# Optimization experiments

Measured on AMD Instinct MI355X. Metric: run time of the kernel, lower is better.

The kernel has to match this reference:

```python
import jax, jax.numpy as jnp
import numpy as np

N_E = 4096
E_DIM = 512
BETA = 0.25


def setup_inputs() -> dict:
    key = jax.random.key(0)
    k1, k2 = jax.random.split(key)
    z = jax.random.normal(k1, (32, 512, E_DIM), dtype=jnp.float32)
    # embedding.weight ~ U(-1/n_e, 1/n_e)
    emb = jax.random.uniform(k2, (N_E, E_DIM), dtype=jnp.float32,
                             minval=-1.0 / N_E, maxval=1.0 / N_E)
    return {"z": z, "emb": emb}


def reference(z, emb):
    B, S, D = z.shape
    zf = z.reshape(-1, D)  # (N, D)
    # squared L2 distances: ||z||^2 + ||e||^2 - 2 z @ e^T  -> (N, n_e)
    d = (jnp.sum(zf * zf, axis=1, keepdims=True)
         + jnp.sum(emb * emb, axis=1)
         - 2.0 * jnp.matmul(zf, emb.T))
    idx = jnp.argmin(d, axis=1)  # (N,)
    z_q = emb[idx].reshape(z.shape)

    # commitment / codebook loss (detach = stop_gradient)
    loss = (jnp.mean((z_q - jax.lax.stop_gradient(z)) ** 2)
            + BETA * jnp.mean((jax.lax.stop_gradient(z_q) - z) ** 2))

    # straight-through estimator
    z_q_st = z + jax.lax.stop_gradient(z_q - z)

    # perplexity via codeword usage histogram (equiv. to mean of one-hots)
    N = zf.shape[0]
    counts = jnp.zeros((N_E,), dtype=z.dtype).at[idx].add(1.0)
    e_mean = counts / N
    perplexity = jnp.exp(-jnp.sum(e_mean * jnp.log(e_mean + 1e-10)))

    return (loss, z_q_st, idx, perplexity)
```

## Files before the change

kernel.cpp:

```cpp
#include <hip/hip_runtime.h>
#include <math.h>

#define NROWS 16384
#define DDIM  512
#define NE    4096
#define NZ    (NROWS * DDIM)
#define MAXC  32
#define MARGIN 2e-3f

typedef __attribute__((ext_vector_type(8))) short bf16x8;
typedef __attribute__((ext_vector_type(4))) float f32x4;

__device__ __forceinline__ float sqr_rn(float x) { return __fmul_rn(x, x); }
__device__ __forceinline__ ushort f2bf(float f) {
    const unsigned u = __float_as_uint(f);
    return (ushort)((u + 0x7fffu + ((u >> 16) & 1u)) >> 16);
}
__device__ __forceinline__ unsigned pack2(float a, float b) {
    return (unsigned)f2bf(a) | ((unsigned)f2bf(b) << 16);
}

__global__ void k_prepZ(const float* __restrict__ z, ushort* __restrict__ zh,
                        float* __restrict__ znorm) {
    const int t = blockIdx.x * blockDim.x + threadIdx.x;
    const int row = t >> 2, blk = t & 3;
    const float4* p = (const float4*)(z + (size_t)row * DDIM + blk * 128);
    ushort* zo = zh + (size_t)row * DDIM + blk * 128;
    float4 v0 = p[0], v1 = p[1];
    {
        uint4 w; w.x = pack2(v0.x, v0.y); w.y = pack2(v0.z, v0.w);
        w.z = pack2(v1.x, v1.y); w.w = pack2(v1.z, v1.w);
        *(uint4*)zo = w;
    }
    float r[8];
    r[0] = sqr_rn(v0.x); r[1] = sqr_rn(v0.y); r[2] = sqr_rn(v0.z); r[3] = sqr_rn(v0.w);
    r[4] = sqr_rn(v1.x); r[5] = sqr_rn(v1.y); r[6] = sqr_rn(v1.z); r[7] = sqr_rn(v1.w);
    #pragma unroll
    for (int i = 1; i < 16; ++i) {
        v0 = p[2 * i]; v1 = p[2 * i + 1];
        uint4 w; w.x = pack2(v0.x, v0.y); w.y = pack2(v0.z, v0.w);
        w.z = pack2(v1.x, v1.y); w.w = pack2(v1.z, v1.w);
        *(uint4*)(zo + i * 8) = w;
        r[0] = __fadd_rn(r[0], sqr_rn(v0.x)); r[1] = __fadd_rn(r[1], sqr_rn(v0.y));
        r[2] = __fadd_rn(r[2], sqr_rn(v0.z)); r[3] = __fadd_rn(r[3], sqr_rn(v0.w));
        r[4] = __fadd_rn(r[4], sqr_rn(v1.x)); r[5] = __fadd_rn(r[5], sqr_rn(v1.y));
        r[6] = __fadd_rn(r[6], sqr_rn(v1.z)); r[7] = __fadd_rn(r[7], sqr_rn(v1.w));
    }
    const float B = __fadd_rn(__fadd_rn(__fadd_rn(r[0], r[1]), __fadd_rn(r[2], r[3])),
                              __fadd_rn(__fadd_rn(r[4], r[5]), __fadd_rn(r[6], r[7])));
    const float s01 = __fadd_rn(B, __shfl_xor(B, 1));
    const float zn  = __fadd_rn(s01, __shfl_xor(s01, 2));
    if (blk == 0) znorm[row] = zn;
}

__global__ void k_prepE(const float* __restrict__ emb, ushort* __restrict__ eh,
                        float* __restrict__ bnorm, unsigned* __restrict__ counts) {
    const int lane = threadIdx.x & 63;
    const int c = (blockIdx.x * blockDim.x + threadIdx.x) >> 6;
    const float4* p = (const float4*)(emb + (size_t)c * DDIM);
    const float4 v0 = p[lane * 2], v1 = p[lane * 2 + 1];
    uint4 w; w.x = pack2(v0.x, v0.y); w.y = pack2(v0.z, v0.w);
    w.z = pack2(v1.x, v1.y); w.w = pack2(v1.z, v1.w);
    *(uint4*)(eh + (size_t)c * DDIM + lane * 8) = w;
    float s = v0.x*v0.x + v0.y*v0.y + v0.z*v0.z + v0.w*v0.w
            + v1.x*v1.x + v1.y*v1.y + v1.z*v1.z + v1.w*v1.w;
    #pragma unroll
    for (int m = 32; m; m >>= 1) s += __shfl_xor(s, m);
    if (lane == 0) { bnorm[c] = s; counts[c] = 0u; }
}

__global__ __launch_bounds__(256) void k_mfma(const ushort* __restrict__ zh,
                                              const ushort* __restrict__ eh,
                                              const float* __restrict__ bnorm,
                                              ushort* __restrict__ sbuf) {
    __shared__ ushort Af[8 * 512];
    __shared__ ushort Bf[8 * 512];
    const int tid = threadIdx.x;
    const int lane = tid & 63;
    const int w = tid >> 6;
    const int wrow = (w >> 1) * 64, wcol = (w & 1) * 64;
    const int rbase = blockIdx.x * 128, cbase = blockIdx.y * 128;
    const int sr = tid >> 1, sh = tid & 1;
    const int g  = sr >> 4, r15 = sr & 15;
    const int r16 = lane & 15, g4 = (lane >> 4) * 4;

    f32x4 acc[4][4];
    #pragma unroll
    for (int i = 0; i < 4; ++i)
        #pragma unroll
        for (int j = 0; j < 4; ++j) acc[i][j] = (f32x4){0.f, 0.f, 0.f, 0.f};

    for (int kb = 0; kb < DDIM; kb += 32) {
        const ushort* ga = zh + (size_t)(rbase + sr) * DDIM + kb + sh * 16;
        const ushort* gb = eh + (size_t)(cbase + sr) * DDIM + kb + sh * 16;
        const uint4 qa0 = *(const uint4*)ga;
        const uint4 qa1 = *(const uint4*)(ga + 8);
        const uint4 qb0 = *(const uint4*)gb;
        const uint4 qb1 = *(const uint4*)(gb + 8);
        __syncthreads();
        {
            ushort* pa = &Af[g * 512 + r15 * 8 + sh * 4];
            *(uint2*)(pa +   0) = make_uint2(qa0.x, qa0.y);
            *(uint2*)(pa + 128) = make_uint2(qa0.z, qa0.w);
            *(uint2*)(pa + 256) = make_uint2(qa1.x, qa1.y);
            *(uint2*)(pa + 384) = make_uint2(qa1.z, qa1.w);
            ushort* pb = &Bf[g * 512 + r15 * 8 + sh * 4];
            *(uint2*)(pb +   0) = make_uint2(qb0.x, qb0.y);
            *(uint2*)(pb + 128) = make_uint2(qb0.z, qb0.w);
            *(uint2*)(pb + 256) = make_uint2(qb1.x, qb1.y);
            *(uint2*)(pb + 384) = make_uint2(qb1.z, qb1.w);
        }
        __syncthreads();
        bf16x8 af[4], bf[4];
        #pragma unroll
        for (int f = 0; f < 4; ++f) {
            af[f] = *(const bf16x8*)&Af[((wrow >> 4) + f) * 512 + lane * 8];
            bf[f] = *(const bf16x8*)&Bf[((wcol >> 4) + f) * 512 + lane * 8];
        }
        #pragma unroll
        for (int fi = 0; fi < 4; ++fi)
            #pragma unroll
            for (int fj = 0; fj < 4; ++fj)
                acc[fi][fj] = __builtin_amdgcn_mfma_f32_16x16x32_bf16(
                    af[fi], bf[fj], acc[fi][fj], 0, 0, 0);
    }

    float bn[4];
    #pragma unroll
    for (int fj = 0; fj < 4; ++fj) bn[fj] = bnorm[cbase + wcol + fj * 16 + r16];

    #pragma unroll
    for (int fi = 0; fi < 4; ++fi) {
        #pragma unroll
        for (int r = 0; r < 4; ++r) {
            const int row = rbase + wrow + fi * 16 + g4 + r;
            float s[4];
            #pragma unroll
            for (int fj = 0; fj < 4; ++fj) s[fj] = fmaf(-2.f, acc[fi][fj][r], bn[fj]);
            uint2* sp = (uint2*)(sbuf + (size_t)row * NE + cbase + wcol);
            sp[r16] = make_uint2(pack2(s[0], s[1]), pack2(s[2], s[3]));
        }
    }
}

__device__ __forceinline__ unsigned long long exact_key(const float4* __restrict__ zp4,
                                                        const float* __restrict__ emb,
                                                        const float* __restrict__ bnorm,
                                                        float zn, int c) {
    const float4* ep4 = (const float4*)(emb + (size_t)c * DDIM);
    float acc = 0.f;
    #pragma unroll 8
    for (int q = 0; q < DDIM / 4; ++q) {
        const float4 zv = zp4[q];
        const float4 ev = ep4[q];
        acc = fmaf(zv.x, ev.x, acc);
        acc = fmaf(zv.y, ev.y, acc);
        acc = fmaf(zv.z, ev.z, acc);
        acc = fmaf(zv.w, ev.w, acc);
    }
    const float s = __fsub_rn(__fadd_rn(zn, bnorm[c]), __fmul_rn(2.f, acc));
    return ((unsigned long long)__float_as_uint(s) << 32) | (unsigned)c;
}

__global__ void k_pick(const ushort* __restrict__ sbuf, const float* __restrict__ z,
                       const float* __restrict__ emb, const float* __restrict__ znorm,
                       const float* __restrict__ bnorm, int* __restrict__ idxbuf) {
    __shared__ unsigned candL[4][MAXC];
    __shared__ unsigned cntL[4];
    const int lane = threadIdx.x & 63;
    const int w = threadIdx.x >> 6;
    const int row = blockIdx.x * 4 + w;
    if (threadIdx.x < 4) cntL[threadIdx.x] = 0u;
    __syncthreads();

    const uint4* p = (const uint4*)(sbuf + (size_t)row * NE);
    uint4 v[8];
    #pragma unroll
    for (int j = 0; j < 8; ++j) v[j] = p[j * 64 + lane];
    float mn = INFINITY;
    #pragma unroll
    for (int j = 0; j < 8; ++j) {
        const unsigned* u = (const unsigned*)&v[j];
        #pragma unroll
        for (int q = 0; q < 4; ++q) {
            mn = fminf(mn, __uint_as_float(u[q] << 16));
            mn = fminf(mn, __uint_as_float(u[q] & 0xffff0000u));
        }
    }
    #pragma unroll
    for (int m = 32; m; m >>= 1) mn = fminf(mn, __shfl_xor(mn, m));
    const float thr = mn + MARGIN;
    #pragma unroll
    for (int j = 0; j < 8; ++j) {
        const unsigned* u = (const unsigned*)&v[j];
        #pragma unroll
        for (int q = 0; q < 4; ++q) {
            #pragma unroll
            for (int hi = 0; hi < 2; ++hi) {
                const float val = __uint_as_float(hi ? (u[q] & 0xffff0000u) : (u[q] << 16));
                if (val <= thr) {
                    const int pos = j * 512 + lane * 8 + q * 2 + hi;
                    const int inb = pos & 63;
                    const int col = (pos >> 6) * 64 + (inb & 3) * 16 + (inb >> 2);
                    const unsigned slot = atomicAdd(&cntL[w], 1u);
                    if (slot < MAXC) candL[w][slot] = (unsigned)col;
                }
            }
        }
    }
    __syncthreads();

    const int cnt = (int)cntL[w];
    int id;
    if (cnt == 1) {
        id = (int)(candL[w][0] & (NE - 1));
    } else {
        const float zn = znorm[row];
        const float4* zp4 = (const float4*)(z + (size_t)row * DDIM);
        unsigned long long best = ~0ULL;
        if (cnt >= 2 && cnt <= MAXC) {
            if (lane < cnt)
                best = exact_key(zp4, emb, bnorm, zn, (int)(candL[w][lane] & (NE - 1)));
        } else {
            for (int c = lane; c < NE; c += 64) {
                const unsigned long long k = exact_key(zp4, emb, bnorm, zn, c);
                if (k < best) best = k;
            }
        }
        #pragma unroll
        for (int m = 32; m; m >>= 1) {
            const unsigned long long ov = __shfl_xor(best, m);
            if (ov < best) best = ov;
        }
        id = (int)(__shfl(best, 0) & (unsigned long long)(NE - 1));
    }
    if (lane == 0) idxbuf[row] = id;
}

__global__ void k_gather(const int* __restrict__ idxbuf, const float* __restrict__ z,
                         const float* __restrict__ emb, float* __restrict__ out,
                         unsigned* __restrict__ counts, float* __restrict__ d2buf) {
    const int lane = threadIdx.x & 63;
    const int row = blockIdx.x * 4 + (threadIdx.x >> 6);
    const int id = idxbuf[row] & (NE - 1);
    const float* zp = z + (size_t)row * DDIM;
    const float* ep = emb + (size_t)id * DDIM;
    float* op = out + 1 + (size_t)row * DDIM;
    float d2 = 0.f;
    #pragma unroll
    for (int m = 0; m < 8; ++m) {
        const int k = m * 64 + lane;
        const float e = ep[k];
        const float zv = zp[k];
        const float t = e - zv;
        op[k] = zv + t;
        d2 = fmaf(t, t, d2);
    }
    #pragma unroll
    for (int m = 32; m; m >>= 1) d2 += __shfl_xor(d2, m);
    if (lane == 0) {
        atomicAdd(&counts[id], 1u);
        d2buf[row] = d2;
        out[1 + (size_t)NZ + row] = (float)id;
    }
}

__global__ void k_final(const float* __restrict__ d2buf, const unsigned* __restrict__ counts,
                        float* __restrict__ out) {
    __shared__ double sh[256];
    __shared__ float  shf[256];
    const int tid = threadIdx.x;
    double ent = 0.0;
    for (int i = tid; i < NE; i += 256) {
        const double p = (double)counts[i] / (double)NROWS;
        ent += p * log(p + 1e-10);
    }
    float sse = 0.f;
    for (int i = tid; i < NROWS; i += 256) sse += d2buf[i];
    sh[tid] = ent; shf[tid] = sse;
    __syncthreads();
    for (int s = 128; s; s >>= 1) {
        if (tid < s) { sh[tid] += sh[tid + s]; shf[tid] += shf[tid + s]; }
        __syncthreads();
    }
    if (tid == 0) {
        out[0] = 1.25f * (shf[0] / (float)NZ);
        out[1 + (size_t)NZ + NROWS] = (float)exp(-sh[0]);
    }
}

extern "C" void kernel_launch(void* const* d_in, const int* in_sizes, int n_in,
                              void* d_out, int out_size, void* d_ws, size_t ws_size,
                              hipStream_t stream) {
    const float* z   = (const float*)d_in[0];
    const float* emb = (const float*)d_in[1];
    float* out = (float*)d_out;
    char* ws = (char*)d_ws;

    ushort* zh = (ushort*)(out + 4);
    ushort* eh = (ushort*)(out + 4 + 4194304);

    size_t off = 0;
    float*    bnorm  = (float*)(ws + off); off += (size_t)NE * 4;
    unsigned* counts = (unsigned*)(ws + off); off += (size_t)NE * 4;
    float*    d2buf  = (float*)(ws + off); off += (size_t)NROWS * 4;
    float*    znorm  = (float*)(ws + off); off += (size_t)NROWS * 4;
    int*      idxbuf = (int*)(ws + off); off += (size_t)NROWS * 4;
    ushort*   sbuf   = (ushort*)(ws + off);

    k_prepZ<<<256, 256, 0, stream>>>(z, zh, znorm);
    k_prepE<<<1024, 256, 0, stream>>>(emb, eh, bnorm, counts);
    k_mfma<<<dim3(NROWS / 128, NE / 128), 256, 0, stream>>>(zh, eh, bnorm, sbuf);
    k_pick<<<NROWS / 4, 256, 0, stream>>>(sbuf, z, emb, znorm, bnorm, idxbuf);
    k_gather<<<NROWS / 4, 256, 0, stream>>>(idxbuf, z, emb, out, counts, d2buf);
    k_final<<<1, 256, 0, stream>>>(d2buf, counts, out);
}
```

Before: 296.3 us.

## Fuse prep kernels, use global_load_lds in MFMA, add block-min guided pick

Merges the z and codebook prep kernels into one launch and fuses pick with gather, which drops the idx buffer round trip. The MFMA kernel now loads tiles straight from global memory into LDS with global_load_lds instead of staging them through registers. It also writes a per-row, per-64-column block minimum, so the pick kernel only rescans blocks within the margin instead of reading the whole bf16 score row. This adds extra writes and shuffles in the MFMA epilogue, raises the candidate cap to 64, and falls back to the old path when the workspace is too small.

```diff
diff --git a/kernel.cpp b/kernel.cpp
--- a/kernel.cpp
+++ b/kernel.cpp
@@ -5,7 +5,7 @@
 #define DDIM  512
 #define NE    4096
 #define NZ    (NROWS * DDIM)
-#define MAXC  32
+#define MAXC  64
 #define MARGIN 2e-3f
 
 typedef __attribute__((ext_vector_type(8))) short bf16x8;
@@ -19,60 +19,68 @@
 __device__ __forceinline__ unsigned pack2(float a, float b) {
     return (unsigned)f2bf(a) | ((unsigned)f2bf(b) << 16);
 }
-
-__global__ void k_prepZ(const float* __restrict__ z, ushort* __restrict__ zh,
-                        float* __restrict__ znorm) {
-    const int t = blockIdx.x * blockDim.x + threadIdx.x;
-    const int row = t >> 2, blk = t & 3;
-    const float4* p = (const float4*)(z + (size_t)row * DDIM + blk * 128);
-    ushort* zo = zh + (size_t)row * DDIM + blk * 128;
-    float4 v0 = p[0], v1 = p[1];
-    {
+__device__ __forceinline__ void glds16(const void* g, void* l) {
+    __builtin_amdgcn_global_load_lds(
+        (const __attribute__((address_space(1))) unsigned int*)g,
+        (__attribute__((address_space(3))) unsigned int*)l, 16, 0, 0);
+}
+
+__global__ void k_prep(const float* __restrict__ z, const float* __restrict__ emb,
+                       ushort* __restrict__ zh, ushort* __restrict__ eh,
+                       float* __restrict__ znorm, float* __restrict__ bnorm,
+                       unsigned* __restrict__ counts) {
+    if (blockIdx.x < 1024) {
+        const int lane = threadIdx.x & 63;
+        const int c = (int)((blockIdx.x * 256 + threadIdx.x) >> 6);
+        const float4* p = (const float4*)(emb + (size_t)c * DDIM);
+        const float4 v0 = p[lane * 2], v1 = p[lane * 2 + 1];
         uint4 w; w.x = pack2(v0.x, v0.y); w.y = pack2(v0.z, v0.w);
         w.z = pack2(v1.x, v1.y); w.w = pack2(v1.z, v1.w);
-        *(uint4*)zo = w;
-    }
-    float r[8];
-    r[0] = sqr_rn(v0.x); r[1] = sqr_rn(v0.y); r[2] = sqr_rn(v0.z); r[3] = sqr_rn(v0.w);
-    r[4] = sqr_rn(v1.x); r[5] = sqr_rn(v1.y); r[6] = sqr_rn(v1.z); r[7] = sqr_rn(v1.w);
-    #pragma unroll
-    for (int i = 1; i < 16; ++i) {
-        v0 = p[2 * i]; v1 = p[2 * i + 1];
-        uint4 w; w.x = pack2(v0.x, v0.y); w.y = pack2(v0.z, v0.w);
-        w.z = pack2(v1.x, v1.y); w.w = pack2(v1.z, v1.w);
-        *(uint4*)(zo + i * 8) = w;
-        r[0] = __fadd_rn(r[0], sqr_rn(v0.x)); r[1] = __fadd_rn(r[1], sqr_rn(v0.y));
-        r[2] = __fadd_rn(r[2], sqr_rn(v0.z)); r[3] = __fadd_rn(r[3], sqr_rn(v0.w));
-        r[4] = __fadd_rn(r[4], sqr_rn(v1.x)); r[5] = __fadd_rn(r[5], sqr_rn(v1.y));
-        r[6] = __fadd_rn(r[6], sqr_rn(v1.z)); r[7] = __fadd_rn(r[7], sqr_rn(v1.w));
-    }
-    const float B = __fadd_rn(__fadd_rn(__fadd_rn(r[0], r[1]), __fadd_rn(r[2], r[3])),
-                              __fadd_rn(__fadd_rn(r[4], r[5]), __fadd_rn(r[6], r[7])));
-    const float s01 = __fadd_rn(B, __shfl_xor(B, 1));
-    const float zn  = __fadd_rn(s01, __shfl_xor(s01, 2));
-    if (blk == 0) znorm[row] = zn;
-}
-
-__global__ void k_prepE(const float* __restrict__ emb, ushort* __restrict__ eh,
-                        float* __restrict__ bnorm, unsigned* __restrict__ counts) {
-    const int lane = threadIdx.x & 63;
-    const int c = (blockIdx.x * blockDim.x + threadIdx.x) >> 6;
-    const float4* p = (const float4*)(emb + (size_t)c * DDIM);
-    const float4 v0 = p[lane * 2], v1 = p[lane * 2 + 1];
-    uint4 w; w.x = pack2(v0.x, v0.y); w.y = pack2(v0.z, v0.w);
-    w.z = pack2(v1.x, v1.y); w.w = pack2(v1.z, v1.w);
-    *(uint4*)(eh + (size_t)c * DDIM + lane * 8) = w;
-    float s = v0.x*v0.x + v0.y*v0.y + v0.z*v0.z + v0.w*v0.w
-            + v1.x*v1.x + v1.y*v1.y + v1.z*v1.z + v1.w*v1.w;
-    #pragma unroll
-    for (int m = 32; m; m >>= 1) s += __shfl_xor(s, m);
-    if (lane == 0) { bnorm[c] = s; counts[c] = 0u; }
-}
-
+        *(uint4*)(eh + (size_t)c * DDIM + lane * 8) = w;
+        float s = v0.x*v0.x + v0.y*v0.y + v0.z*v0.z + v0.w*v0.w
+                + v1.x*v1.x + v1.y*v1.y + v1.z*v1.z + v1.w*v1.w;
+        #pragma unroll
+        for (int m = 32; m; m >>= 1) s += __shfl_xor(s, m);
+        if (lane == 0) { bnorm[c] = s; counts[c] = 0u; }
+    } else {
+        const int t = (int)((blockIdx.x - 1024) * 256 + threadIdx.x);
+        const int row = t >> 2, blk = t & 3;
+        const float4* p = (const float4*)(z + (size_t)row * DDIM + blk * 128);
+        ushort* zo = zh + (size_t)row * DDIM + blk * 128;
+        float4 v0 = p[0], v1 = p[1];
+        {
+            uint4 w; w.x = pack2(v0.x, v0.y); w.y = pack2(v0.z, v0.w);
+            w.z = pack2(v1.x, v1.y); w.w = pack2(v1.z, v1.w);
+            *(uint4*)zo = w;
+        }
+        float r[8];
+        r[0] = sqr_rn(v0.x); r[1] = sqr_rn(v0.y); r[2] = sqr_rn(v0.z); r[3] = sqr_rn(v0.w);
+        r[4] = sqr_rn(v1.x); r[5] = sqr_rn(v1.y); r[6] = sqr_rn(v1.z); r[7] = sqr_rn(v1.w);
+        #pragma unroll
+        for (int i = 1; i < 16; ++i) {
+            v0 = p[2 * i]; v1 = p[2 * i + 1];
+            uint4 w; w.x = pack2(v0.x, v0.y); w.y = pack2(v0.z, v0.w);
+            w.z = pack2(v1.x, v1.y); w.w = pack2(v1.z, v1.w);
+            *(uint4*)(zo + i * 8) = w;
+            r[0] = __fadd_rn(r[0], sqr_rn(v0.x)); r[1] = __fadd_rn(r[1], sqr_rn(v0.y));
+            r[2] = __fadd_rn(r[2], sqr_rn(v0.z)); r[3] = __fadd_rn(r[3], sqr_rn(v0.w));
+            r[4] = __fadd_rn(r[4], sqr_rn(v1.x)); r[5] = __fadd_rn(r[5], sqr_rn(v1.y));
+            r[6] = __fadd_rn(r[6], sqr_rn(v1.z)); r[7] = __fadd_rn(r[7], sqr_rn(v1.w));
+        }
+        const float B = __fadd_rn(__fadd_rn(__fadd_rn(r[0], r[1]), __fadd_rn(r[2], r[3])),
+                                  __fadd_rn(__fadd_rn(r[4], r[5]), __fadd_rn(r[6], r[7])));
+        const float s01 = __fadd_rn(B, __shfl_xor(B, 1));
+        const float zn  = __fadd_rn(s01, __shfl_xor(s01, 2));
+        if (blk == 0) znorm[row] = zn;
+    }
+}
+
+template <int USE_BLK>
 __global__ __launch_bounds__(256) void k_mfma(const ushort* __restrict__ zh,
                                               const ushort* __restrict__ eh,
                                               const float* __restrict__ bnorm,
-                                              ushort* __restrict__ sbuf) {
+                                              ushort* __restrict__ sbuf,
+                                              float* __restrict__ rowblkmin) {
     __shared__ ushort Af[8 * 512];
     __shared__ ushort Bf[8 * 512];
     const int tid = threadIdx.x;
@@ -80,9 +88,16 @@
     const int w = tid >> 6;
     const int wrow = (w >> 1) * 64, wcol = (w & 1) * 64;
     const int rbase = blockIdx.x * 128, cbase = blockIdx.y * 128;
-    const int sr = tid >> 1, sh = tid & 1;
-    const int g  = sr >> 4, r15 = sr & 15;
     const int r16 = lane & 15, g4 = (lane >> 4) * 4;
+    const int k8 = (lane >> 4) * 8;
+    const int c0 = 2 * w, c1 = c0 + 1;
+
+    const ushort* gA0 = zh + (size_t)(rbase + 16 * c0 + r16) * DDIM + k8;
+    const ushort* gA1 = zh + (size_t)(rbase + 16 * c1 + r16) * DDIM + k8;
+    const ushort* gB0 = eh + (size_t)(cbase + 16 * c0 + r16) * DDIM + k8;
+    const ushort* gB1 = eh + (size_t)(cbase + 16 * c1 + r16) * DDIM + k8;
+    ushort* lA0 = &Af[c0 * 512]; ushort* lA1 = &Af[c1 * 512];
+    ushort* lB0 = &Bf[c0 * 512]; ushort* lB1 = &Bf[c1 * 512];
 
     f32x4 acc[4][4];
     #pragma unroll
@@ -91,25 +106,11 @@
         for (int j = 0; j < 4; ++j) acc[i][j] = (f32x4){0.f, 0.f, 0.f, 0.f};
 
     for (int kb = 0; kb < DDIM; kb += 32) {
-        const ushort* ga = zh + (size_t)(rbase + sr) * DDIM + kb + sh * 16;
-        const ushort* gb = eh + (size_t)(cbase + sr) * DDIM + kb + sh * 16;
-        const uint4 qa0 = *(const uint4*)ga;
-        const uint4 qa1 = *(const uint4*)(ga + 8);
-        const uint4 qb0 = *(const uint4*)gb;
-        const uint4 qb1 = *(const uint4*)(gb + 8);
         __syncthreads();
-        {
-            ushort* pa = &Af[g * 512 + r15 * 8 + sh * 4];
-            *(uint2*)(pa +   0) = make_uint2(qa0.x, qa0.y);
-            *(uint2*)(pa + 128) = make_uint2(qa0.z, qa0.w);
-            *(uint2*)(pa + 256) = make_uint2(qa1.x, qa1.y);
-            *(uint2*)(pa + 384) = make_uint2(qa1.z, qa1.w);
-            ushort* pb = &Bf[g * 512 + r15 * 8 + sh * 4];
-            *(uint2*)(pb +   0) = make_uint2(qb0.x, qb0.y);
-            *(uint2*)(pb + 128) = make_uint2(qb0.z, qb0.w);
-            *(uint2*)(pb + 256) = make_uint2(qb1.x, qb1.y);
-            *(uint2*)(pb + 384) = make_uint2(qb1.z, qb1.w);
-        }
+        glds16(gA0 + kb, lA0);
+        glds16(gA1 + kb, lA1);
+        glds16(gB0 + kb, lB0);
+        glds16(gB1 + kb, lB1);
         __syncthreads();
         bf16x8 af[4], bf[4];
         #pragma unroll
@@ -139,6 +140,13 @@
             for (int fj = 0; fj < 4; ++fj) s[fj] = fmaf(-2.f, acc[fi][fj][r], bn[fj]);
             uint2* sp = (uint2*)(sbuf + (size_t)row * NE + cbase + wcol);
             sp[r16] = make_uint2(pack2(s[0], s[1]), pack2(s[2], s[3]));
+            if (USE_BLK) {
+                float m = fminf(fminf(s[0], s[1]), fminf(s[2], s[3]));
+                #pragma unroll
+                for (int x = 1; x < 16; x <<= 1) m = fminf(m, __shfl_xor(m, x));
+                if (r16 == 0)
+                    rowblkmin[(size_t)row * 64 + blockIdx.y * 2 + (w & 1)] = m;
+            }
         }
     }
 }
@@ -162,10 +170,13 @@
     return ((unsigned long long)__float_as_uint(s) << 32) | (unsigned)c;
 }
 
-__global__ void k_pick(const ushort* __restrict__ sbuf, const float* __restrict__ z,
-                       const float* __restrict__ emb, const float* __restrict__ znorm,
-                       const float* __restrict__ bnorm, int* __restrict__ idxbuf) {
-    __shared__ unsigned candL[4][MAXC];
+template <int GUIDED>
+__global__ void k_pg(const ushort* __restrict__ sbuf, const float* __restrict__ rowblkmin,
+                     const float* __restrict__ z, const float* __restrict__ emb,
+                     const float* __restrict__ znorm, const float* __restrict__ bnorm,
+                     float* __restrict__ out, unsigned* __restrict__ counts,
+                     float* __restrict__ d2buf) {
+    __shared__ int candL[4][MAXC];
     __shared__ unsigned cntL[4];
     const int lane = threadIdx.x & 63;
     const int w = threadIdx.x >> 6;
@@ -173,37 +184,57 @@
     if (threadIdx.x < 4) cntL[threadIdx.x] = 0u;
     __syncthreads();
 
-    const uint4* p = (const uint4*)(sbuf + (size_t)row * NE);
-    uint4 v[8];
-    #pragma unroll
-    for (int j = 0; j < 8; ++j) v[j] = p[j * 64 + lane];
-    float mn = INFINITY;
-    #pragma unroll
-    for (int j = 0; j < 8; ++j) {
-        const unsigned* u = (const unsigned*)&v[j];
-        #pragma unroll
-        for (int q = 0; q < 4; ++q) {
-            mn = fminf(mn, __uint_as_float(u[q] << 16));
-            mn = fminf(mn, __uint_as_float(u[q] & 0xffff0000u));
-        }
-    }
-    #pragma unroll
-    for (int m = 32; m; m >>= 1) mn = fminf(mn, __shfl_xor(mn, m));
-    const float thr = mn + MARGIN;
-    #pragma unroll
-    for (int j = 0; j < 8; ++j) {
-        const unsigned* u = (const unsigned*)&v[j];
-        #pragma unroll
-        for (int q = 0; q < 4; ++q) {
+    if (GUIDED) {
+        const float bm = rowblkmin[(size_t)row * 64 + lane];
+        float gmin = bm;
+        #pragma unroll
+        for (int m = 32; m; m >>= 1) gmin = fminf(gmin, __shfl_xor(gmin, m));
+        const float thr = gmin + MARGIN;
+        unsigned long long bmask = __ballot(bm <= thr);
+        while (bmask) {
+            const int b = __builtin_ctzll(bmask); bmask &= bmask - 1;
+            const float val = __uint_as_float(
+                (unsigned)sbuf[(size_t)row * NE + b * 64 + lane] << 16);
+            if (val <= thr) {
+                const unsigned slot = atomicAdd(&cntL[w], 1u);
+                if (slot < MAXC)
+                    candL[w][slot] = b * 64 + (lane & 3) * 16 + (lane >> 2);
+            }
+        }
+    } else {
+        const uint4* p = (const uint4*)(sbuf + (size_t)row * NE);
+        uint4 v[8];
+        #pragma unroll
+        for (int j = 0; j < 8; ++j) v[j] = p[j * 64 + lane];
+        float mn = INFINITY;
+        #pragma unroll
+        for (int j = 0; j < 8; ++j) {
+            const unsigned* u = (const unsigned*)&v[j];
             #pragma unroll
-            for (int hi = 0; hi < 2; ++hi) {
-                const float val = __uint_as_float(hi ? (u[q] & 0xffff0000u) : (u[q] << 16));
-                if (val <= thr) {
-                    const int pos = j * 512 + lane * 8 + q * 2 + hi;
-                    const int inb = pos & 63;
-                    const int col = (pos >> 6) * 64 + (inb & 3) * 16 + (inb >> 2);
-                    const unsigned slot = atomicAdd(&cntL[w], 1u);
-                    if (slot < MAXC) candL[w][slot] = (unsigned)col;
+            for (int q = 0; q < 4; ++q) {
+                mn = fminf(mn, __uint_as_float(u[q] << 16));
+                mn = fminf(mn, __uint_as_float(u[q] & 0xffff0000u));
+            }
+        }
+        #pragma unroll
+        for (int m = 32; m; m >>= 1) mn = fminf(mn, __shfl_xor(mn, m));
+        const float thr = mn + MARGIN;
+        #pragma unroll
+        for (int j = 0; j < 8; ++j) {
+            const unsigned* u = (const unsigned*)&v[j];
+            #pragma unroll
+            for (int q = 0; q < 4; ++q) {
+                #pragma unroll
+                for (int hi = 0; hi < 2; ++hi) {
+                    const float val = __uint_as_float(hi ? (u[q] & 0xffff0000u)
+                                                        : (u[q] << 16));
+                    if (val <= thr) {
+                        const int pos = j * 512 + lane * 8 + q * 2 + hi;
+                        const int inb = pos & 63;
+                        const unsigned slot = atomicAdd(&cntL[w], 1u);
+                        if (slot < MAXC)
+                            candL[w][slot] = (pos >> 6) * 64 + (inb & 3) * 16 + (inb >> 2);
+                    }
                 }
             }
         }
@@ -213,14 +244,14 @@
     const int cnt = (int)cntL[w];
     int id;
     if (cnt == 1) {
-        id = (int)(candL[w][0] & (NE - 1));
+        id = candL[w][0] & (NE - 1);
     } else {
         const float zn = znorm[row];
         const float4* zp4 = (const float4*)(z + (size_t)row * DDIM);
         unsigned long long best = ~0ULL;
         if (cnt >= 2 && cnt <= MAXC) {
             if (lane < cnt)
-                best = exact_key(zp4, emb, bnorm, zn, (int)(candL[w][lane] & (NE - 1)));
+                best = exact_key(zp4, emb, bnorm, zn, candL[w][lane] & (NE - 1));
         } else {
             for (int c = lane; c < NE; c += 64) {
                 const unsigned long long k = exact_key(zp4, emb, bnorm, zn, c);
@@ -234,15 +265,7 @@
         }
         id = (int)(__shfl(best, 0) & (unsigned long long)(NE - 1));
     }
-    if (lane == 0) idxbuf[row] = id;
-}
-
-__global__ void k_gather(const int* __restrict__ idxbuf, const float* __restrict__ z,
-                         const float* __restrict__ emb, float* __restrict__ out,
-                         unsigned* __restrict__ counts, float* __restrict__ d2buf) {
-    const int lane = threadIdx.x & 63;
-    const int row = blockIdx.x * 4 + (threadIdx.x >> 6);
-    const int id = idxbuf[row] & (NE - 1);
+
     const float* zp = z + (size_t)row * DDIM;
     const float* ep = emb + (size_t)id * DDIM;
     float* op = out + 1 + (size_t)row * DDIM;
@@ -305,13 +328,17 @@
     unsigned* counts = (unsigned*)(ws + off); off += (size_t)NE * 4;
     float*    d2buf  = (float*)(ws + off); off += (size_t)NROWS * 4;
     float*    znorm  = (float*)(ws + off); off += (size_t)NROWS * 4;
-    int*      idxbuf = (int*)(ws + off); off += (size_t)NROWS * 4;
-    ushort*   sbuf   = (ushort*)(ws + off);
-
-    k_prepZ<<<256, 256, 0, stream>>>(z, zh, znorm);
-    k_prepE<<<1024, 256, 0, stream>>>(emb, eh, bnorm, counts);
-    k_mfma<<<dim3(NROWS / 128, NE / 128), 256, 0, stream>>>(zh, eh, bnorm, sbuf);
-    k_pick<<<NROWS / 4, 256, 0, stream>>>(sbuf, z, emb, znorm, bnorm, idxbuf);
-    k_gather<<<NROWS / 4, 256, 0, stream>>>(idxbuf, z, emb, out, counts, d2buf);
+    ushort*   sbuf   = (ushort*)(ws + off); off += (size_t)NROWS * NE * 2;
+    float*    rowblkmin = (float*)(ws + off); off += (size_t)NROWS * 64 * 4;
+    const bool guided = ws_size >= off;
+
+    k_prep<<<1280, 256, 0, stream>>>(z, emb, zh, eh, znorm, bnorm, counts);
+    if (guided) {
+        k_mfma<1><<<dim3(NROWS / 128, NE / 128), 256, 0, stream>>>(zh, eh, bnorm, sbuf, rowblkmin);
+        k_pg<1><<<NROWS / 4, 256, 0, stream>>>(sbuf, rowblkmin, z, emb, znorm, bnorm, out, counts, d2buf);
+    } else {
+        k_mfma<0><<<dim3(NROWS / 128, NE / 128), 256, 0, stream>>>(zh, eh, bnorm, sbuf, rowblkmin);
+        k_pg<0><<<NROWS / 4, 256, 0, stream>>>(sbuf, rowblkmin, z, emb, znorm, bnorm, out, counts, d2buf);
+    }
     k_final<<<1, 256, 0, stream>>>(d2buf, counts, out);
 }
```

Measured after the change: 292.7 us. No clear change (-1.2%).
